# Kernel optimization log

Measured on AMD Instinct MI355X. Metric: run time of the kernel, lower is better.

## Reference

```python
import jax, jax.numpy as jnp
import numpy as np

B, N, E = 16, 10000, 320000
C_IN, C_OUT, K = 32, 64, 3
C = C_IN + C_OUT          # 96, channels into each diffusion conv
L = 2 * K - 1             # 5 Chebyshev terms (bidirectional, remove_ln=False)


def setup_inputs() -> dict:
    key = jax.random.key(0)
    ks = jax.random.split(key, 8)
    x = jax.random.normal(ks[0], (B, N, C_IN), dtype=jnp.float32)
    hidden_state = jax.random.normal(ks[1], (B, N, C_OUT), dtype=jnp.float32)
    edge_index = jax.random.randint(ks[2], (2, E), 0, N, dtype=jnp.int64)
    edge_weight = jax.random.uniform(ks[3], (E,), dtype=jnp.float32)
    # xavier-uniform style scale for params
    s_ru = float(np.sqrt(6.0 / (L * C + 2 * C_OUT)))
    s_c = float(np.sqrt(6.0 / (L * C + C_OUT)))
    ru_param = jax.random.uniform(ks[4], (L * C, 2 * C_OUT), minval=-s_ru, maxval=s_ru, dtype=jnp.float32)
    ru_bias = jnp.zeros((2 * C_OUT,), dtype=jnp.float32)
    c_param = jax.random.uniform(ks[5], (L * C, C_OUT), minval=-s_c, maxval=s_c, dtype=jnp.float32)
    c_bias = jnp.zeros((C_OUT,), dtype=jnp.float32)
    return {"x": x, "hidden_state": hidden_state, "edge_index": edge_index,
            "edge_weight": edge_weight, "ru_param": ru_param, "ru_bias": ru_bias,
            "c_param": c_param, "c_bias": c_bias}


def _propagate(h, src, dst, w, num_nodes):
    # gather x_j at src, weight, scatter-add at dst: out[i] = sum_{e: dst=i} w_e * h[src_e]
    return jax.ops.segment_sum(h[src] * w[:, None], dst, num_segments=num_nodes)


def _cheb_conv(x, src, dst, wf, wb, param, bias, k):
    # x: [B, N, C] -> [N, B*C] as in torch transpose(0,1).view(N, B*C)
    b, n, c = x.shape
    xt = jnp.transpose(x, (1, 0, 2)).reshape(n, b * c)
    x0f = xt
    x0b = xt
    x1f = _propagate(xt, src, dst, wf, n)
    x1b = _propagate(xt, dst, src, wb, n)
    outs = [xt, x1f, x1b]
    for _ in range(2, k):
        x2f = 2.0 * _propagate(x1f, src, dst, wf, n) - x0f
        outs.append(x2f)
        x0f, x1f = x1f, x2f
        x2b = 2.0 * _propagate(x1b, dst, src, wb, n) - x0b
        outs.append(x2b)
        x0b, x1b = x1b, x2b
    out = jnp.stack(outs, axis=2)            # [N, B*C, L]
    out = out.reshape(n * b, -1)             # [N*B, C*L] (row-major matches torch view)
    out = out @ param                        # [N*B, out_channels]
    out = jnp.transpose(out.reshape(n, b, -1), (1, 0, 2))  # [B, N, out]
    return out + bias


def reference(x, hidden_state, edge_index, edge_weight, ru_param, ru_bias, c_param, c_bias):
    src, dst = edge_index[0], edge_index[1]
    n = x.shape[1]
    deg_f = jax.ops.segment_sum(edge_weight, src, num_segments=n)
    wf = edge_weight / deg_f[src]            # forward-diffusion normalized weights
    deg_b = jax.ops.segment_sum(edge_weight, dst, num_segments=n)
    wb = edge_weight / deg_b[dst]            # reverse-diffusion normalized weights

    x_and_state = jnp.concatenate([x, hidden_state], axis=2)
    ru = jax.nn.sigmoid(_cheb_conv(x_and_state, src, dst, wf, wb, ru_param, ru_bias, K))
    r = ru[:, :, :C_OUT]
    u = ru[:, :, C_OUT:]
    xrh = jnp.concatenate([x, r * hidden_state], axis=-1)
    # original applies tanh twice
    c = jnp.tanh(jnp.tanh(_cheb_conv(xrh, src, dst, wf, wb, c_param, c_bias, K)))
    return u * hidden_state + (1.0 - u) * c
```

## Files before the change

kernel.cpp:

```cpp
#include <hip/hip_runtime.h>
#include <stdint.h>
#include <stddef.h>

#define Bn    16
#define Nn    10000
#define En    320000
#define CIN   32
#define COUTn 64
#define CCn   96
#define WROWU 768
#define RHU   512
#define MROWS 160000
#define GDEG  (En / 256)
#define GX0   (Nn * WROWU / 256)

typedef __attribute__((ext_vector_type(8))) short short8;
typedef __attribute__((ext_vector_type(4))) float f32x4;
typedef __attribute__((ext_vector_type(2))) float f32x2;
typedef __attribute__((ext_vector_type(4))) unsigned int uint4v;

#if __has_builtin(__builtin_amdgcn_global_load_lds)
#define HAVE_GLL 1
typedef __attribute__((address_space(3))) unsigned char lds_u8;
typedef __attribute__((address_space(1))) const unsigned char glb_u8;
__device__ __forceinline__ void gll16(const void* g, void* l) {
  __builtin_amdgcn_global_load_lds((glb_u8*)g, (lds_u8*)l, 16, 0, 0);
}
#else
#define HAVE_GLL 0
#endif

__device__ __forceinline__ float bflo(unsigned int p) { return __uint_as_float(p << 16); }
__device__ __forceinline__ float bfhi(unsigned int p) { return __uint_as_float(p & 0xffff0000u); }
__device__ __forceinline__ float bf2f(unsigned short u) { return __uint_as_float(((unsigned int)u) << 16); }
__device__ __forceinline__ unsigned int f2bfbits(float f) {
  unsigned int x = __float_as_uint(f);
  return (x + 0x7fffu + ((x >> 16) & 1u)) >> 16;
}
__device__ __forceinline__ unsigned int pack2(float lo, float hi) {
  return f2bfbits(lo) | (f2bfbits(hi) << 16);
}

__global__ void detect_idx(const int* __restrict__ idx, int* __restrict__ flag) {
  int t = threadIdx.x;
  int v = idx[1 + 2 * t];
  unsigned long long bal = __ballot(v != 0);
  if (t == 0) flag[0] = (bal == 0ULL) ? 1 : 0;
}

__device__ __forceinline__ int gidx(const int* __restrict__ p, int i, int is64) {
  return is64 ? p[2 * (long long)i] : p[i];
}

__global__ void deg_x0_wt(const int* __restrict__ idx, const float* __restrict__ w,
                          float* __restrict__ deg_f, float* __restrict__ deg_b,
                          int* __restrict__ cnt_f, int* __restrict__ cnt_b,
                          const int* __restrict__ flag,
                          const float* __restrict__ x, const float* __restrict__ h,
                          unsigned int* __restrict__ X0,
                          const float* __restrict__ ru_p, const float* __restrict__ c_p,
                          unsigned short* __restrict__ Wt1, unsigned short* __restrict__ Wt2) {
  int blk = blockIdx.x;
  if (blk < GDEG) {
    int e = blk * 256 + threadIdx.x;
    int is64 = flag[0];
    if (e < En) {
      int s = gidx(idx, e, is64);
      int d = gidx(idx, En + e, is64);
      float we = w[e];
      atomicAdd(&deg_f[s], we);
      atomicAdd(&deg_b[d], we);
      atomicAdd(&cnt_f[d], 1);
      atomicAdd(&cnt_b[s], 1);
    }
  } else if (blk < GDEG + GX0) {
    long long p = (long long)(blk - GDEG) * 256 + threadIdx.x;
    int node = (int)(p / WROWU);
    int rem = (int)(p % WROWU);
    int b = rem / 48;
    int ci = (rem % 48) * 2;
    float lo, hi;
    if (ci < CIN) {
      const float* s = x + ((size_t)b * Nn + node) * CIN + ci;
      lo = s[0]; hi = s[1];
    } else {
      const float* s = h + ((size_t)b * Nn + node) * COUTn + (ci - CIN);
      lo = s[0]; hi = s[1];
    }
    X0[p] = pack2(lo, hi);
  } else {
    int i = (blk - GDEG - GX0) * 256 + threadIdx.x;
    if (i < 128 * 480) {
      int n = i / 480, k = i % 480;
      int t = k / 96, kk = k % 96;
      float v;
      if (t == 0) v = ru_p[(kk * 5 + 0) * 128 + n] - ru_p[(kk * 5 + 3) * 128 + n] - ru_p[(kk * 5 + 4) * 128 + n];
      else        v = ru_p[(kk * 5 + t) * 128 + n];
      Wt1[i] = (unsigned short)f2bfbits(v);
    }
    if (i < 64 * 480) {
      int n = i / 480, k = i % 480;
      int t = k / 96, kk = k % 96;
      float v;
      if (t == 0) v = c_p[(kk * 5 + 0) * 64 + n] - c_p[(kk * 5 + 3) * 64 + n] - c_p[(kk * 5 + 4) * 64 + n];
      else        v = c_p[(kk * 5 + t) * 64 + n];
      Wt2[i] = (unsigned short)f2bfbits(v);
    }
  }
}

__global__ void exscan_two(const int* __restrict__ cnt_f, const int* __restrict__ cnt_b,
                           int* __restrict__ rp_f, int* __restrict__ rp_b,
                           int* __restrict__ cur_f, int* __restrict__ cur_b, int n) {
  const int* cnt = (blockIdx.x == 0) ? cnt_f : cnt_b;
  int* rp  = (blockIdx.x == 0) ? rp_f  : rp_b;
  int* cur = (blockIdx.x == 0) ? cur_f : cur_b;
  __shared__ int sh[256];
  int t = threadIdx.x;
  int CH = (n + 255) / 256;
  int s0 = t * CH;
  int s1 = s0 + CH; if (s1 > n) s1 = n;
  int s = 0;
  for (int i = s0; i < s1; ++i) s += cnt[i];
  sh[t] = s;
  __syncthreads();
  for (int off = 1; off < 256; off <<= 1) {
    int x = (t >= off) ? sh[t - off] : 0;
    __syncthreads();
    sh[t] += x;
    __syncthreads();
  }
  int run = sh[t] - s;
  for (int i = s0; i < s1; ++i) {
    rp[i] = run; cur[i] = run; run += cnt[i];
  }
  if (t == 255) rp[n] = sh[255];
}

__global__ void fill_csr(const int* __restrict__ idx, const float* __restrict__ w,
                         const float* __restrict__ deg_f, const float* __restrict__ deg_b,
                         int* __restrict__ cur_f, int* __restrict__ cur_b,
                         uint2* __restrict__ cwf, uint2* __restrict__ cwb,
                         const int* __restrict__ flag) {
  int e = blockIdx.x * 256 + threadIdx.x;
  int is64 = flag[0];
  if (e < En) {
    int s = gidx(idx, e, is64);
    int d = gidx(idx, En + e, is64);
    float we = w[e];
    int pf = atomicAdd(&cur_f[d], 1);
    cwf[pf] = make_uint2((unsigned int)s, __float_as_uint(we / deg_f[s]));
    int pb = atomicAdd(&cur_b[s], 1);
    cwb[pb] = make_uint2((unsigned int)d, __float_as_uint(we / deg_b[d]));
  }
}

template<int RU4, int ACT, int EPW>
__device__ __forceinline__ void prop_rowX(const uint4v* __restrict__ in,
                                          uint4v* __restrict__ out,
                                          const int* __restrict__ rp,
                                          const uint2* __restrict__ cw,
                                          int row, int slice, int lane, float alpha) {
  constexpr int GSZ = 64 / EPW;
  constexpr unsigned RB = (unsigned)RU4 * 16u;
  int grp = (EPW == 2) ? (lane >> 5) : (lane >> 4);
  int lg = lane & (GSZ - 1);
  int lgc = (lg < ACT) ? lg : 0;
  unsigned laneByte = (unsigned)(slice * ACT + lgc) * 16u;
  const char* __restrict__ inB = (const char*)in;
  int jb = __builtin_amdgcn_readfirstlane(rp[row]);
  int je = __builtin_amdgcn_readfirstlane(rp[row + 1]);
  int len = je - jb;

  f32x2 a0 = {0.f, 0.f}, a1 = {0.f, 0.f}, a2 = {0.f, 0.f}, a3 = {0.f, 0.f};

  constexpr int STEP = 4 * EPW;
  int i = jb;
  int eM = jb + (len / STEP) * STEP;
  for (; i < eM; i += STEP) {
    #pragma unroll
    for (int k = 0; k < 4; ++k) {
      unsigned int col; float w;
      {
        uint2 e0 = cw[i + k * EPW + 0];
        uint2 e1 = cw[i + k * EPW + 1];
        col = (grp & 1) ? e1.x : e0.x;
        w = __uint_as_float((grp & 1) ? e1.y : e0.y);
        if (EPW == 4) {
          uint2 e2 = cw[i + k * EPW + 2];
          uint2 e3 = cw[i + k * EPW + 3];
          unsigned int colB = (grp & 1) ? e3.x : e2.x;
          float wB = __uint_as_float((grp & 1) ? e3.y : e2.y);
          col = (grp & 2) ? colB : col;
          w = (grp & 2) ? wB : w;
        }
      }
      unsigned off = __umul24(col, RB) + laneByte;
      uint4v q = *(const uint4v*)(inB + off);
      f32x2 wv = {w, w};
      f32x2 v0 = {bflo(q.x), bfhi(q.x)};
      f32x2 v1 = {bflo(q.y), bfhi(q.y)};
      f32x2 v2 = {bflo(q.z), bfhi(q.z)};
      f32x2 v3 = {bflo(q.w), bfhi(q.w)};
      a0 += wv * v0; a1 += wv * v1; a2 += wv * v2; a3 += wv * v3;
    }
  }
  for (; i < je; i += EPW) {
    unsigned int col; float w;
    {
      uint2 e0 = cw[i + 0];
      uint2 e1 = cw[(i + 1 < je) ? i + 1 : i];
      col = (grp & 1) ? e1.x : e0.x;
      w = __uint_as_float((grp & 1) ? e1.y : e0.y);
      if (EPW == 4) {
        uint2 e2 = cw[(i + 2 < je) ? i + 2 : i];
        uint2 e3 = cw[(i + 3 < je) ? i + 3 : i];
        unsigned int colB = (grp & 1) ? e3.x : e2.x;
        float wB = __uint_as_float((grp & 1) ? e3.y : e2.y);
        col = (grp & 2) ? colB : col;
        w = (grp & 2) ? wB : w;
      }
    }
    if (i + grp >= je) w = 0.f;
    unsigned off = __umul24(col, RB) + laneByte;
    uint4v q = *(const uint4v*)(inB + off);
    f32x2 wv = {w, w};
    f32x2 v0 = {bflo(q.x), bfhi(q.x)};
    f32x2 v1 = {bflo(q.y), bfhi(q.y)};
    f32x2 v2 = {bflo(q.z), bfhi(q.z)};
    f32x2 v3 = {bflo(q.w), bfhi(q.w)};
    a0 += wv * v0; a1 += wv * v1; a2 += wv * v2; a3 += wv * v3;
  }

  if (EPW == 4) {
    a0.x += __shfl_xor(a0.x, 16); a0.y += __shfl_xor(a0.y, 16);
    a1.x += __shfl_xor(a1.x, 16); a1.y += __shfl_xor(a1.y, 16);
    a2.x += __shfl_xor(a2.x, 16); a2.y += __shfl_xor(a2.y, 16);
    a3.x += __shfl_xor(a3.x, 16); a3.y += __shfl_xor(a3.y, 16);
  }
  a0.x += __shfl_xor(a0.x, 32); a0.y += __shfl_xor(a0.y, 32);
  a1.x += __shfl_xor(a1.x, 32); a1.y += __shfl_xor(a1.y, 32);
  a2.x += __shfl_xor(a2.x, 32); a2.y += __shfl_xor(a2.y, 32);
  a3.x += __shfl_xor(a3.x, 32); a3.y += __shfl_xor(a3.y, 32);

  if (grp == 0 && lg < ACT) {
    uint4v o;
    o.x = pack2(alpha * a0.x, alpha * a0.y);
    o.y = pack2(alpha * a1.x, alpha * a1.y);
    o.z = pack2(alpha * a2.x, alpha * a2.y);
    o.w = pack2(alpha * a3.x, alpha * a3.y);
    out[(size_t)row * RU4 + slice * ACT + lg] = o;
  }
}

template<int RU4, int ACT, int EPW>
__launch_bounds__(256)
__global__ void prop_dualX(const uint4v* __restrict__ in,
                           uint4v* __restrict__ outF, uint4v* __restrict__ outB,
                           const int* __restrict__ rp_f, const uint2* __restrict__ cwf,
                           const int* __restrict__ rp_b, const uint2* __restrict__ cwb) {
  int lane = threadIdx.x & 63;
  int wave = threadIdx.x >> 6;
  int slice = blockIdx.x & 7;
  int row = ((blockIdx.x >> 3) << 2) + wave;
  prop_rowX<RU4, ACT, EPW>(in, outF, rp_f, cwf, row, slice, lane, 1.f);
  prop_rowX<RU4, ACT, EPW>(in, outB, rp_b, cwb, row, slice, lane, 1.f);
}

template<int RU4, int ACT, int EPW>
__launch_bounds__(256)
__global__ void prop_ckX(const uint4v* __restrict__ in, uint4v* __restrict__ out,
                         const int* __restrict__ rp, const uint2* __restrict__ cw,
                         float alpha) {
  int lane = threadIdx.x & 63;
  int wave = threadIdx.x >> 6;
  int slice = blockIdx.x & 7;
  int row = ((blockIdx.x >> 3) << 2) + wave;
  prop_rowX<RU4, ACT, EPW>(in, out, rp, cw, row, slice, lane, alpha);
}

struct Msrc {
  const uint4* xs[5];
  const uint4* rh[5];
};

template<int NT, int MODE>
__device__ __forceinline__ void gemm_body(int blk, Msrc g, int nterms, int t0,
                          const unsigned short* __restrict__ Wt,
                          const float* __restrict__ bias,
                          float* __restrict__ outp,
                          unsigned short* __restrict__ rh0_s,
                          unsigned short* __restrict__ U_out,
                          const unsigned short* __restrict__ U_in,
                          const float* __restrict__ hglob) {
  constexpr int NJ = NT / 16;
  __shared__ __align__(16) unsigned short As[128 * 96];
  __shared__ __align__(16) unsigned short Bs[NT * 96];

  int m0 = blk * 128;
  int tid = threadIdx.x;
  int wave = tid >> 6;
  int lane = tid & 63;
  int quad = lane >> 4;
  int lm = lane & 15;
  int wm = wave * 32;
  int nodeBase = m0 >> 4;

  f32x4 acc[2][NJ];
  #pragma unroll
  for (int i = 0; i < 2; ++i)
    #pragma unroll
    for (int j = 0; j < NJ; ++j) acc[i][j] = (f32x4){0.f, 0.f, 0.f, 0.f};

  for (int t = 0; t < nterms; ++t) {
    const uint4* xs4 = g.xs[t];
    const uint4* rh4 = g.rh[t];
    if (rh4 == nullptr) {
      const uint4* src = xs4 + (size_t)m0 * 12;
#if HAVE_GLL
      #pragma unroll
      for (int it = 0; it < 6; ++it) {
        int q = tid + it * 256;
        gll16(src + q, (char*)As + (q & ~63) * 16);
      }
#else
      #pragma unroll
      for (int it = 0; it < 6; ++it) {
        int q = tid + it * 256;
        uint4 v = src[q];
        *(uint4*)&As[q * 8] = v;
      }
#endif
    } else {
      #pragma unroll
      for (int it = 0; it < 6; ++it) {
        int q = tid + it * 256;
        int row = q / 12, slot = q % 12;
        int node = nodeBase + (row >> 4);
        int b = row & 15;
        uint4 v;
        if (slot < 4) v = xs4[(size_t)node * 192 + b * 12 + slot];
        else          v = rh4[(size_t)node * 128 + b * 8 + (slot - 4)];
        *(uint4*)&As[q * 8] = v;
      }
    }
#if HAVE_GLL
    #pragma unroll
    for (int it = 0; it < NT * 12 / 256; ++it) {
      int q = tid + it * 256;
      int n = q / 12, slot = q % 12;
      gll16(Wt + (size_t)n * 480 + (t0 + t) * 96 + slot * 8, (char*)Bs + (q & ~63) * 16);
    }
#else
    for (int q = tid; q < NT * 12; q += 256) {
      int n = q / 12, slot = q % 12;
      uint4 v = *(const uint4*)(Wt + (size_t)n * 480 + (t0 + t) * 96 + slot * 8);
      *(uint4*)&Bs[q * 8] = v;
    }
#endif
    __syncthreads();

    #pragma unroll
    for (int k32 = 0; k32 < 3; ++k32) {
      int kb = k32 * 32 + quad * 8;
      short8 a0 = *(const short8*)&As[(wm + lm) * 96 + kb];
      short8 a1 = *(const short8*)&As[(wm + 16 + lm) * 96 + kb];
      #pragma unroll
      for (int j = 0; j < NJ; ++j) {
        short8 bf = *(const short8*)&Bs[(j * 16 + lm) * 96 + kb];
        acc[0][j] = __builtin_amdgcn_mfma_f32_16x16x32_bf16(a0, bf, acc[0][j], 0, 0, 0);
        acc[1][j] = __builtin_amdgcn_mfma_f32_16x16x32_bf16(a1, bf, acc[1][j], 0, 0, 0);
      }
    }
    __syncthreads();
  }

  #pragma unroll
  for (int i = 0; i < 2; ++i) {
    #pragma unroll
    for (int j = 0; j < NJ; ++j) {
      int col = j * 16 + lm;
      #pragma unroll
      for (int r = 0; r < 4; ++r) {
        int row = m0 + wm + i * 16 + quad * 4 + r;
        int node = row >> 4, b = row & 15;
        float v = acc[i][j][r];
        if (MODE == 0) {
          float s = 1.f / (1.f + expf(-(bias[col] + v)));
          if (col < COUTn) {
            float hv = hglob[((size_t)b * Nn + node) * COUTn + col];
            rh0_s[(size_t)row * 64 + col] = (unsigned short)f2bfbits(s * hv);
          } else {
            U_out[(size_t)row * 64 + (col - COUTn)] = (unsigned short)f2bfbits(s);
          }
        } else if (MODE == 1) {
          outp[((size_t)b * Nn + node) * COUTn + col] = bias[col] + v;
        } else {
          size_t oa = ((size_t)b * Nn + node) * COUTn + col;
          float cp = outp[oa] + v;
          float c = tanhf(tanhf(cp));
          float u = bf2f(U_in[(size_t)row * 64 + col]);
          outp[oa] = u * hglob[oa] + (1.f - u) * c;
        }
      }
    }
  }
}

template<int NT, int MODE>
__launch_bounds__(256)
__global__ void gemm_mfma(Msrc g, int nterms, int t0,
                          const unsigned short* __restrict__ Wt,
                          const float* __restrict__ bias,
                          float* __restrict__ outp,
                          unsigned short* __restrict__ rh0_s,
                          unsigned short* __restrict__ U_out,
                          const unsigned short* __restrict__ U_in,
                          const float* __restrict__ hglob) {
  gemm_body<NT, MODE>(blockIdx.x, g, nterms, t0, Wt, bias, outp, rh0_s, U_out, U_in, hglob);
}

__launch_bounds__(256)
__global__ void fused_g2a(Msrc g,
                          const unsigned short* __restrict__ Wt,
                          const float* __restrict__ bias,
                          float* __restrict__ outp,
                          const uint4v* __restrict__ inF, uint4v* __restrict__ outF,
                          const int* __restrict__ rp_f, const uint2* __restrict__ cwf,
                          const uint4v* __restrict__ inB, uint4v* __restrict__ outB,
                          const int* __restrict__ rp_b, const uint2* __restrict__ cwb) {
  int b = blockIdx.x;
  if (b < 1256) {
    if (b < 1250)
      gemm_body<64, 1>(b, g, 3, 0, Wt, bias, outp, nullptr, nullptr, nullptr, nullptr);
    return;
  }
  int lane = threadIdx.x & 63;
  int wave = threadIdx.x >> 6;
  if (b < 21256) {
    int b2 = b - 1256;
    prop_rowX<128, 16, 4>(inF, outF, rp_f, cwf, ((b2 >> 3) << 2) + wave, b2 & 7, lane, 2.f);
  } else {
    int b2 = b - 21256;
    prop_rowX<128, 16, 4>(inB, outB, rp_b, cwb, ((b2 >> 3) << 2) + wave, b2 & 7, lane, 2.f);
  }
}

extern "C" void kernel_launch(void* const* d_in, const int* in_sizes, int n_in,
                              void* d_out, int out_size, void* d_ws, size_t ws_size,
                              hipStream_t stream) {
  const float* x   = (const float*)d_in[0];
  const float* h   = (const float*)d_in[1];
  const int*   idx = (const int*)d_in[2];
  const float* ew  = (const float*)d_in[3];
  const float* ru_param = (const float*)d_in[4];
  const float* ru_bias  = (const float*)d_in[5];
  const float* c_param  = (const float*)d_in[6];
  const float* c_bias   = (const float*)d_in[7];
  float* outp = (float*)d_out;
  (void)in_sizes; (void)n_in; (void)out_size;

  char* ws = (char*)d_ws;
  size_t off = 0;
  auto alloc = [&](size_t bytes) -> char* {
    char* p = ws + off;
    off += (bytes + 255) & ~(size_t)255;
    return p;
  };

  float* deg_f = (float*)alloc(40960);
  float* deg_b = (float*)alloc(40960);
  int*   cnt_f = (int*)alloc(40960);
  int*   cnt_b = (int*)alloc(40960);
  int*   rp_f  = (int*)alloc((Nn + 1) * sizeof(int));
  int*   rp_b  = (int*)alloc((Nn + 1) * sizeof(int));
  int*   cur_f = (int*)alloc(Nn * sizeof(int));
  int*   cur_b = (int*)alloc(Nn * sizeof(int));
  int*   flag  = (int*)alloc(256);
  uint2* cwf   = (uint2*)alloc((size_t)En * 8);
  uint2* cwb   = (uint2*)alloc((size_t)En * 8);
  unsigned short* Wt1 = (unsigned short*)alloc(128 * 480 * 2);
  unsigned short* Wt2 = (unsigned short*)alloc(64 * 480 * 2);

  unsigned int* A0   = (unsigned int*)alloc((size_t)Nn * WROWU * 4);
  unsigned int* T1f  = (unsigned int*)alloc((size_t)Nn * WROWU * 4);
  unsigned int* T1b  = (unsigned int*)alloc((size_t)Nn * WROWU * 4);
  unsigned int* T2f  = (unsigned int*)alloc((size_t)Nn * WROWU * 4);
  unsigned int* T2b  = (unsigned int*)alloc((size_t)Nn * WROWU * 4);
  unsigned int* rh0  = (unsigned int*)alloc((size_t)Nn * RHU * 4);
  unsigned int* rh1f = (unsigned int*)alloc((size_t)Nn * RHU * 4);
  unsigned int* rh1b = (unsigned int*)alloc((size_t)Nn * RHU * 4);
  unsigned int* Ubuf = (unsigned int*)alloc((size_t)Nn * RHU * 4);
  unsigned int* rh2fN = (unsigned int*)alloc((size_t)Nn * RHU * 4);
  unsigned int* rh2bN = (unsigned int*)alloc((size_t)Nn * RHU * 4);
  bool bigws = (off <= ws_size);

  hipMemsetAsync(ws, 0, 4 * 40960, stream);
  detect_idx<<<1, 64, 0, stream>>>(idx, flag);
  deg_x0_wt<<<GDEG + GX0 + 240, 256, 0, stream>>>(
      idx, ew, deg_f, deg_b, cnt_f, cnt_b, flag,
      x, h, A0, ru_param, c_param, Wt1, Wt2);
  exscan_two<<<2, 256, 0, stream>>>(cnt_f, cnt_b, rp_f, rp_b, cur_f, cur_b, Nn);
  fill_csr<<<En / 256, 256, 0, stream>>>(idx, ew, deg_f, deg_b, cur_f, cur_b,
                                         cwf, cwb, flag);

  const int gP = (Nn / 4) * 8;

  prop_dualX<192, 24, 2><<<gP, 256, 0, stream>>>(
      (const uint4v*)A0, (uint4v*)T1f, (uint4v*)T1b, rp_f, cwf, rp_b, cwb);
  prop_ckX<192, 24, 2><<<gP, 256, 0, stream>>>(
      (const uint4v*)T1f, (uint4v*)T2f, rp_f, cwf, 2.f);
  prop_ckX<192, 24, 2><<<gP, 256, 0, stream>>>(
      (const uint4v*)T1b, (uint4v*)T2b, rp_b, cwb, 2.f);

  Msrc g1;
  g1.xs[0] = (const uint4*)A0;  g1.rh[0] = nullptr;
  g1.xs[1] = (const uint4*)T1f; g1.rh[1] = nullptr;
  g1.xs[2] = (const uint4*)T1b; g1.rh[2] = nullptr;
  g1.xs[3] = (const uint4*)T2f; g1.rh[3] = nullptr;
  g1.xs[4] = (const uint4*)T2b; g1.rh[4] = nullptr;
  gemm_mfma<128, 0><<<MROWS / 128, 256, 0, stream>>>(
      g1, 5, 0, Wt1, ru_bias, nullptr,
      (unsigned short*)rh0, (unsigned short*)Ubuf, nullptr, h);

  prop_dualX<128, 16, 4><<<gP, 256, 0, stream>>>(
      (const uint4v*)rh0, (uint4v*)rh1f, (uint4v*)rh1b, rp_f, cwf, rp_b, cwb);

  Msrc g2a;
  g2a.xs[0] = (const uint4*)A0;  g2a.rh[0] = (const uint4*)rh0;
  g2a.xs[1] = (const uint4*)T1f; g2a.rh[1] = (const uint4*)rh1f;
  g2a.xs[2] = (const uint4*)T1b; g2a.rh[2] = (const uint4*)rh1b;
  g2a.xs[3] = nullptr; g2a.rh[3] = nullptr;
  g2a.xs[4] = nullptr; g2a.rh[4] = nullptr;

  const uint4* g2b_rh0;
  const uint4* g2b_rh1;
  if (bigws) {
    fused_g2a<<<41256, 256, 0, stream>>>(
        g2a, Wt2, c_bias, outp,
        (const uint4v*)rh1f, (uint4v*)rh2fN, rp_f, cwf,
        (const uint4v*)rh1b, (uint4v*)rh2bN, rp_b, cwb);
    g2b_rh0 = (const uint4*)rh2fN;
    g2b_rh1 = (const uint4*)rh2bN;
  } else {
    gemm_mfma<64, 1><<<MROWS / 128, 256, 0, stream>>>(
        g2a, 3, 0, Wt2, c_bias, outp, nullptr, nullptr, nullptr, nullptr);
    prop_ckX<128, 16, 4><<<gP, 256, 0, stream>>>(
        (const uint4v*)rh1f, (uint4v*)rh0, rp_f, cwf, 2.f);
    prop_ckX<128, 16, 4><<<gP, 256, 0, stream>>>(
        (const uint4v*)rh1b, (uint4v*)rh1f, rp_b, cwb, 2.f);
    g2b_rh0 = (const uint4*)rh0;
    g2b_rh1 = (const uint4*)rh1f;
  }

  Msrc g2b;
  g2b.xs[0] = (const uint4*)T2f; g2b.rh[0] = g2b_rh0;
  g2b.xs[1] = (const uint4*)T2b; g2b.rh[1] = g2b_rh1;
  g2b.xs[2] = nullptr; g2b.rh[2] = nullptr;
  g2b.xs[3] = nullptr; g2b.rh[3] = nullptr;
  g2b.xs[4] = nullptr; g2b.rh[4] = nullptr;
  gemm_mfma<64, 2><<<MROWS / 128, 256, 0, stream>>>(
      g2b, 2, 3, Wt2, c_bias, outp, nullptr, nullptr,
      (const unsigned short*)Ubuf, h);
}
```

Measured before the change: 811.5 us.

## Overlap first-conv partial GEMM with second-order propagation in fused kernel

```diff
diff --git a/kernel.cpp b/kernel.cpp
--- a/kernel.cpp
+++ b/kernel.cpp
@@ -292,7 +292,8 @@
                           unsigned short* __restrict__ rh0_s,
                           unsigned short* __restrict__ U_out,
                           const unsigned short* __restrict__ U_in,
-                          const float* __restrict__ hglob) {
+                          const float* __restrict__ hglob,
+                          const float* __restrict__ Pbuf) {
   constexpr int NJ = NT / 16;
   __shared__ __align__(16) unsigned short As[128 * 96];
   __shared__ __align__(16) unsigned short Bs[NT * 96];
@@ -385,7 +386,8 @@
         int row = m0 + wm + i * 16 + quad * 4 + r;
         int node = row >> 4, b = row & 15;
         float v = acc[i][j][r];
-        if (MODE == 0) {
+        if (MODE == 0 || MODE == 4) {
+          if (MODE == 4) v += Pbuf[(size_t)row * 128 + col];
           float s = 1.f / (1.f + expf(-(bias[col] + v)));
           if (col < COUTn) {
             float hv = hglob[((size_t)b * Nn + node) * COUTn + col];
@@ -416,15 +418,101 @@
                           unsigned short* __restrict__ rh0_s,
                           unsigned short* __restrict__ U_out,
                           const unsigned short* __restrict__ U_in,
-                          const float* __restrict__ hglob) {
-  gemm_body<NT, MODE>(blockIdx.x, g, nterms, t0, Wt, bias, outp, rh0_s, U_out, U_in, hglob);
-}
-
-__launch_bounds__(256)
-__global__ void fused_g2a(Msrc g,
+                          const float* __restrict__ hglob,
+                          const float* __restrict__ Pbuf) {
+  gemm_body<NT, MODE>(blockIdx.x, g, nterms, t0, Wt, bias, outp, rh0_s, U_out, U_in, hglob, Pbuf);
+}
+
+template<int NT, int MODE>
+__device__ __forceinline__ void gemm_regA(int blk, Msrc g, int nterms, int t0,
                           const unsigned short* __restrict__ Wt,
                           const float* __restrict__ bias,
-                          float* __restrict__ outp,
+                          float* __restrict__ outp) {
+  constexpr int NJ = NT / 16;
+  __shared__ __align__(16) unsigned short Bs[NT * 96];
+  int m0 = blk * 128;
+  int tid = threadIdx.x;
+  int wave = tid >> 6;
+  int lane = tid & 63;
+  int quad = lane >> 4;
+  int lm = lane & 15;
+  int wm = wave * 32;
+  int r0 = m0 + wm + lm, r1 = r0 + 16;
+
+  f32x4 acc[2][NJ];
+  #pragma unroll
+  for (int i = 0; i < 2; ++i)
+    #pragma unroll
+    for (int j = 0; j < NJ; ++j) acc[i][j] = (f32x4){0.f, 0.f, 0.f, 0.f};
+
+  for (int t = 0; t < nterms; ++t) {
+    const uint4* xs4 = g.xs[t];
+    const uint4* rh4 = g.rh[t];
+#if HAVE_GLL
+    #pragma unroll
+    for (int it = 0; it < NT * 12 / 256; ++it) {
+      int q = tid + it * 256;
+      int n = q / 12, slot = q % 12;
+      gll16(Wt + (size_t)n * 480 + (t0 + t) * 96 + slot * 8, (char*)Bs + (q & ~63) * 16);
+    }
+#else
+    for (int q = tid; q < NT * 12; q += 256) {
+      int n = q / 12, slot = q % 12;
+      *(uint4*)&Bs[q * 8] = *(const uint4*)(Wt + (size_t)n * 480 + (t0 + t) * 96 + slot * 8);
+    }
+#endif
+    __syncthreads();
+
+    #pragma unroll
+    for (int k32 = 0; k32 < 3; ++k32) {
+      int kb = k32 * 32 + quad * 8;
+      int slot = k32 * 4 + quad;
+      uint4 ar0, ar1;
+      if (rh4 == nullptr) {
+        ar0 = xs4[(size_t)r0 * 12 + slot];
+        ar1 = xs4[(size_t)r1 * 12 + slot];
+      } else if (k32 == 0) {
+        ar0 = xs4[(size_t)(r0 >> 4) * 192 + (r0 & 15) * 12 + slot];
+        ar1 = xs4[(size_t)(r1 >> 4) * 192 + (r1 & 15) * 12 + slot];
+      } else {
+        ar0 = rh4[(size_t)(r0 >> 4) * 128 + (r0 & 15) * 8 + (slot - 4)];
+        ar1 = rh4[(size_t)(r1 >> 4) * 128 + (r1 & 15) * 8 + (slot - 4)];
+      }
+      short8 a0 = *(const short8*)&ar0;
+      short8 a1 = *(const short8*)&ar1;
+      #pragma unroll
+      for (int j = 0; j < NJ; ++j) {
+        short8 bf = *(const short8*)&Bs[(j * 16 + lm) * 96 + kb];
+        acc[0][j] = __builtin_amdgcn_mfma_f32_16x16x32_bf16(a0, bf, acc[0][j], 0, 0, 0);
+        acc[1][j] = __builtin_amdgcn_mfma_f32_16x16x32_bf16(a1, bf, acc[1][j], 0, 0, 0);
+      }
+    }
+    __syncthreads();
+  }
+
+  #pragma unroll
+  for (int i = 0; i < 2; ++i) {
+    #pragma unroll
+    for (int j = 0; j < NJ; ++j) {
+      int col = j * 16 + lm;
+      #pragma unroll
+      for (int r = 0; r < 4; ++r) {
+        int row = m0 + wm + i * 16 + quad * 4 + r;
+        float v = acc[i][j][r];
+        if (MODE == 3) {
+          outp[(size_t)row * 128 + col] = v;
+        } else {
+          int node = row >> 4, b = row & 15;
+          outp[((size_t)b * Nn + node) * COUTn + col] = bias[col] + v;
+        }
+      }
+    }
+  }
+}
+
+__launch_bounds__(256)
+__global__ void fused_g1a(Msrc g, const unsigned short* __restrict__ Wt,
+                          float* __restrict__ Pbuf,
                           const uint4v* __restrict__ inF, uint4v* __restrict__ outF,
                           const int* __restrict__ rp_f, const uint2* __restrict__ cwf,
                           const uint4v* __restrict__ inB, uint4v* __restrict__ outB,
@@ -432,7 +520,31 @@
   int b = blockIdx.x;
   if (b < 1256) {
     if (b < 1250)
-      gemm_body<64, 1>(b, g, 3, 0, Wt, bias, outp, nullptr, nullptr, nullptr, nullptr);
+      gemm_regA<128, 3>(b, g, 3, 0, Wt, nullptr, Pbuf);
+    return;
+  }
+  int lane = threadIdx.x & 63;
+  int wave = threadIdx.x >> 6;
+  if (b < 21256) {
+    int b2 = b - 1256;
+    prop_rowX<192, 24, 2>(inF, outF, rp_f, cwf, ((b2 >> 3) << 2) + wave, b2 & 7, lane, 2.f);
+  } else {
+    int b2 = b - 21256;
+    prop_rowX<192, 24, 2>(inB, outB, rp_b, cwb, ((b2 >> 3) << 2) + wave, b2 & 7, lane, 2.f);
+  }
+}
+
+__launch_bounds__(256)
+__global__ void fused_g2a(Msrc g, const unsigned short* __restrict__ Wt,
+                          const float* __restrict__ bias, float* __restrict__ outp,
+                          const uint4v* __restrict__ inF, uint4v* __restrict__ outF,
+                          const int* __restrict__ rp_f, const uint2* __restrict__ cwf,
+                          const uint4v* __restrict__ inB, uint4v* __restrict__ outB,
+                          const int* __restrict__ rp_b, const uint2* __restrict__ cwb) {
+  int b = blockIdx.x;
+  if (b < 1256) {
+    if (b < 1250)
+      gemm_regA<64, 1>(b, g, 3, 0, Wt, bias, outp);
     return;
   }
   int lane = threadIdx.x & 63;
@@ -493,7 +605,11 @@
   unsigned int* Ubuf = (unsigned int*)alloc((size_t)Nn * RHU * 4);
   unsigned int* rh2fN = (unsigned int*)alloc((size_t)Nn * RHU * 4);
   unsigned int* rh2bN = (unsigned int*)alloc((size_t)Nn * RHU * 4);
-  bool bigws = (off <= ws_size);
+  size_t off1 = off;
+  float* Pbuf = (float*)alloc((size_t)MROWS * 128 * sizeof(float));
+  size_t off2 = off;
+  bool ws1 = (off1 <= ws_size);
+  bool ws2 = (off2 <= ws_size);
 
   hipMemsetAsync(ws, 0, 4 * 40960, stream);
   detect_idx<<<1, 64, 0, stream>>>(idx, flag);
@@ -508,10 +624,6 @@
 
   prop_dualX<192, 24, 2><<<gP, 256, 0, stream>>>(
       (const uint4v*)A0, (uint4v*)T1f, (uint4v*)T1b, rp_f, cwf, rp_b, cwb);
-  prop_ckX<192, 24, 2><<<gP, 256, 0, stream>>>(
-      (const uint4v*)T1f, (uint4v*)T2f, rp_f, cwf, 2.f);
-  prop_ckX<192, 24, 2><<<gP, 256, 0, stream>>>(
-      (const uint4v*)T1b, (uint4v*)T2b, rp_b, cwb, 2.f);
 
   Msrc g1;
   g1.xs[0] = (const uint4*)A0;  g1.rh[0] = nullptr;
@@ -519,9 +631,31 @@
   g1.xs[2] = (const uint4*)T1b; g1.rh[2] = nullptr;
   g1.xs[3] = (const uint4*)T2f; g1.rh[3] = nullptr;
   g1.xs[4] = (const uint4*)T2b; g1.rh[4] = nullptr;
-  gemm_mfma<128, 0><<<MROWS / 128, 256, 0, stream>>>(
-      g1, 5, 0, Wt1, ru_bias, nullptr,
-      (unsigned short*)rh0, (unsigned short*)Ubuf, nullptr, h);
+
+  if (ws2) {
+    Msrc g1a = g1;
+    fused_g1a<<<41256, 256, 0, stream>>>(
+        g1a, Wt1, Pbuf,
+        (const uint4v*)T1f, (uint4v*)T2f, rp_f, cwf,
+        (const uint4v*)T1b, (uint4v*)T2b, rp_b, cwb);
+    Msrc g1b;
+    g1b.xs[0] = (const uint4*)T2f; g1b.rh[0] = nullptr;
+    g1b.xs[1] = (const uint4*)T2b; g1b.rh[1] = nullptr;
+    g1b.xs[2] = nullptr; g1b.rh[2] = nullptr;
+    g1b.xs[3] = nullptr; g1b.rh[3] = nullptr;
+    g1b.xs[4] = nullptr; g1b.rh[4] = nullptr;
+    gemm_mfma<128, 4><<<MROWS / 128, 256, 0, stream>>>(
+        g1b, 2, 3, Wt1, ru_bias, nullptr,
+        (unsigned short*)rh0, (unsigned short*)Ubuf, nullptr, h, Pbuf);
+  } else {
+    prop_ckX<192, 24, 2><<<gP, 256, 0, stream>>>(
+        (const uint4v*)T1f, (uint4v*)T2f, rp_f, cwf, 2.f);
+    prop_ckX<192, 24, 2><<<gP, 256, 0, stream>>>(
+        (const uint4v*)T1b, (uint4v*)T2b, rp_b, cwb, 2.f);
+    gemm_mfma<128, 0><<<MROWS / 128, 256, 0, stream>>>(
+        g1, 5, 0, Wt1, ru_bias, nullptr,
+        (unsigned short*)rh0, (unsigned short*)Ubuf, nullptr, h, nullptr);
+  }
 
   prop_dualX<128, 16, 4><<<gP, 256, 0, stream>>>(
       (const uint4v*)rh0, (uint4v*)rh1f, (uint4v*)rh1b, rp_f, cwf, rp_b, cwb);
@@ -535,7 +669,7 @@
 
   const uint4* g2b_rh0;
   const uint4* g2b_rh1;
-  if (bigws) {
+  if (ws1) {
     fused_g2a<<<41256, 256, 0, stream>>>(
         g2a, Wt2, c_bias, outp,
         (const uint4v*)rh1f, (uint4v*)rh2fN, rp_f, cwf,
@@ -544,7 +678,7 @@
     g2b_rh1 = (const uint4*)rh2bN;
   } else {
     gemm_mfma<64, 1><<<MROWS / 128, 256, 0, stream>>>(
-        g2a, 3, 0, Wt2, c_bias, outp, nullptr, nullptr, nullptr, nullptr);
+        g2a, 3, 0, Wt2, c_bias, outp, nullptr, nullptr, nullptr, nullptr, nullptr);
     prop_ckX<128, 16, 4><<<gP, 256, 0, stream>>>(
         (const uint4v*)rh1f, (uint4v*)rh0, rp_f, cwf, 2.f);
     prop_ckX<128, 16, 4><<<gP, 256, 0, stream>>>(
@@ -561,5 +695,5 @@
   g2b.xs[4] = nullptr; g2b.rh[4] = nullptr;
   gemm_mfma<64, 2><<<MROWS / 128, 256, 0, stream>>>(
       g2b, 2, 3, Wt2, c_bias, outp, nullptr, nullptr,
-      (const unsigned short*)Ubuf, h);
-}
+      (const unsigned short*)Ubuf, h, nullptr);
+}
```

After: 819.6 us. About the same (+1.0%).
